# Performance work log

Hardware: AMD Instinct MI355X
Metric: run time of the kernel (lower is better)

The kernel has to match this reference:

```python
import jax, jax.numpy as jnp
import numpy as np

T, D, N, K, H, F = 2048, 4096, 32, 8, 128, 14336
THETA = 500000.0
EPS = 1e-5


def setup_inputs() -> dict:
    key = jax.random.key(0)
    ks = jax.random.split(key, 10)
    s = 0.02  # weight init scale
    return {
        "x": jax.random.normal(ks[0], (T, D), jnp.float32),
        "positions": jnp.arange(T, dtype=jnp.int32),
        "ln1_scale": jnp.ones((D,), jnp.float32),
        "w_q": jax.random.normal(ks[1], (D, N, H), jnp.float32) * s,
        "w_k": jax.random.normal(ks[2], (D, K, H), jnp.float32) * s,
        "w_v": jax.random.normal(ks[3], (D, K, H), jnp.float32) * s,
        "w_o": jax.random.normal(ks[4], (N, H, D), jnp.float32) * s,
        "ln2_scale": jnp.ones((D,), jnp.float32),
        "w_gate": jax.random.normal(ks[5], (D, F), jnp.float32) * s,
        "w_up": jax.random.normal(ks[6], (D, F), jnp.float32) * s,
        "w_down": jax.random.normal(ks[7], (F, D), jnp.float32) * s,
    }


def _rms_norm(x, scale):
    var = jnp.mean(jnp.square(x), axis=-1, keepdims=True)
    return x * jax.lax.rsqrt(var + EPS) * scale


def _apply_rope(x, pos):
    # x: [T, heads, H]; Llama rotate-half RoPE
    half = H // 2
    inv_freq = 1.0 / (THETA ** (jnp.arange(half, dtype=jnp.float32) / half))
    ang = pos.astype(jnp.float32)[:, None] * inv_freq[None, :]      # [T, half]
    cos = jnp.cos(ang)[:, None, :]
    sin = jnp.sin(ang)[:, None, :]
    x1, x2 = x[..., :half], x[..., half:]
    return jnp.concatenate([x1 * cos - x2 * sin, x2 * cos + x1 * sin], axis=-1)


def reference(x, positions, ln1_scale, w_q, w_k, w_v, w_o, ln2_scale, w_gate, w_up, w_down):
    # --- input RMSNorm ---
    h = _rms_norm(x, ln1_scale)
    # --- QKV projections + RoPE ---
    q = _apply_rope(jnp.einsum('td,dnh->tnh', h, w_q), positions)   # [T,N,H]
    k = _apply_rope(jnp.einsum('td,dkh->tkh', h, w_k), positions)   # [T,K,H]
    v = jnp.einsum('td,dkh->tkh', h, w_v)                            # [T,K,H]
    # --- GQA causal attention (prefill) ---
    G = N // K
    qg = q.reshape(T, K, G, H)
    scale = 1.0 / jnp.sqrt(jnp.float32(H))
    scores = jnp.einsum('tkgh,skh->kgts', qg, k) * scale             # [K,G,T,T]
    causal = positions[:, None] >= positions[None, :]                # [T,T]
    scores = jnp.where(causal[None, None], scores, jnp.finfo(scores.dtype).min)
    probs = jax.nn.softmax(scores, axis=-1)
    attn = jnp.einsum('kgts,skh->tkgh', probs, v).reshape(T, N, H)
    attn_out = jnp.einsum('tnh,nhd->td', attn, w_o)
    # --- residual ---
    residual = attn_out + x
    # --- post-attn RMSNorm + SwiGLU MLP ---
    h2 = _rms_norm(residual, ln2_scale)
    gate = jax.nn.silu(h2 @ w_gate)
    up = h2 @ w_up
    out = (gate * up) @ w_down
    return residual + out
```

## Files before the change

### kernel.cpp

```cpp
#include <hip/hip_runtime.h>

typedef __attribute__((ext_vector_type(8))) short bf16x8;
typedef __attribute__((ext_vector_type(4))) float f32x4;

constexpr int T = 2048;
constexpr int D = 4096;
constexpr int NQ = 32;
constexpr int NKV = 8;
constexpr int H = 128;
constexpr int F = 14336;
constexpr int NQKV = (NQ + 2 * NKV) * H;
constexpr int VOFF = (NQ + NKV) * H;

__device__ inline unsigned short f2bf(float f) {
  unsigned u = __float_as_uint(f);
  return (unsigned short)((u + 0x7FFFu + ((u >> 16) & 1u)) >> 16);
}

__device__ inline void gload_lds16(const void* g, void* l) {
  __builtin_amdgcn_global_load_lds((const __attribute__((address_space(1))) void*)g,
                                   (__attribute__((address_space(3))) void*)l, 16, 0, 0);
}

#define MFMA16(a, b, c) __builtin_amdgcn_mfma_f32_16x16x32_bf16(a, b, c, 0, 0, 0)

template <int MODE>
__global__ __launch_bounds__(256) void transpose_bf16(const float* __restrict__ in,
                                                      unsigned short* __restrict__ out,
                                                      int K, int N) {
  __shared__ float tile[64 * 65];
  const int kb = blockIdx.x * 64;
  const int nb = blockIdx.y * 64;
  const int tid = threadIdx.x;
  const int r = tid >> 2;
  const int c4 = tid & 3;
#pragma unroll
  for (int i = 0; i < 4; ++i) {
    float4 v = *(const float4*)(in + (size_t)(kb + r) * N + nb + c4 * 16 + i * 4);
    *(float4*)&tile[r * 65 + c4 * 16 + i * 4] = v;
  }
  __syncthreads();
  const int n = tid >> 2;
  const int kq = tid & 3;
  int nsrc = nb + n;
  int prow = (MODE == 0) ? nsrc : ((nsrc >> 4) * 32 + (nsrc & 15) + (MODE == 2 ? 16 : 0));
#pragma unroll
  for (int half = 0; half < 2; ++half) {
    ushort4 o0, o1;
    int k0 = kq * 16 + half * 8;
    o0.x = f2bf(tile[(k0 + 0) * 65 + n]);
    o0.y = f2bf(tile[(k0 + 1) * 65 + n]);
    o0.z = f2bf(tile[(k0 + 2) * 65 + n]);
    o0.w = f2bf(tile[(k0 + 3) * 65 + n]);
    o1.x = f2bf(tile[(k0 + 4) * 65 + n]);
    o1.y = f2bf(tile[(k0 + 5) * 65 + n]);
    o1.z = f2bf(tile[(k0 + 6) * 65 + n]);
    o1.w = f2bf(tile[(k0 + 7) * 65 + n]);
    unsigned short* op = out + (size_t)prow * K + kb + k0;
    *(ushort4*)(op + 0) = o0;
    *(ushort4*)(op + 4) = o1;
  }
}

__global__ __launch_bounds__(256) void rmsnorm_kernel(
    const float* __restrict__ in, const float* __restrict__ scale,
    unsigned short* __restrict__ out) {
  int row = blockIdx.x;
  const float4* xr = (const float4*)(in + (size_t)row * D);
  const float4* sr = (const float4*)scale;
  float4 vals[4];
  float ss = 0.f;
#pragma unroll
  for (int i = 0; i < 4; ++i) {
    float4 v = xr[threadIdx.x + i * 256];
    vals[i] = v;
    ss += v.x * v.x + v.y * v.y + v.z * v.z + v.w * v.w;
  }
#pragma unroll
  for (int off = 32; off; off >>= 1) ss += __shfl_xor(ss, off, 64);
  __shared__ float wsum[4];
  if ((threadIdx.x & 63) == 0) wsum[threadIdx.x >> 6] = ss;
  __syncthreads();
  float r = rsqrtf((wsum[0] + wsum[1] + wsum[2] + wsum[3]) * (1.f / D) + 1e-5f);
#pragma unroll
  for (int i = 0; i < 4; ++i) {
    int vi = threadIdx.x + i * 256;
    float4 v = vals[i];
    float4 s = sr[vi];
    ushort4 o;
    o.x = f2bf(v.x * r * s.x);
    o.y = f2bf(v.y * r * s.y);
    o.z = f2bf(v.z * r * s.z);
    o.w = f2bf(v.w * r * s.w);
    *(ushort4*)(out + (size_t)row * D + (size_t)vi * 4) = o;
  }
}

__global__ __launch_bounds__(256) void rmsnorm_add3(
    const float* __restrict__ a, const float* __restrict__ b,
    const float* __restrict__ c, const float* __restrict__ scale,
    float* __restrict__ residOut, unsigned short* __restrict__ out) {
  int row = blockIdx.x;
  const float4* ar = (const float4*)(a + (size_t)row * D);
  const float4* br = (const float4*)(b + (size_t)row * D);
  const float4* cr = (const float4*)(c + (size_t)row * D);
  const float4* sr = (const float4*)scale;
  float4* rr = (float4*)(residOut + (size_t)row * D);
  float4 vals[4];
  float ss = 0.f;
#pragma unroll
  for (int i = 0; i < 4; ++i) {
    int vi = threadIdx.x + i * 256;
    float4 va = ar[vi], vb = br[vi], vc = cr[vi];
    float4 v;
    v.x = va.x + vb.x + vc.x;
    v.y = va.y + vb.y + vc.y;
    v.z = va.z + vb.z + vc.z;
    v.w = va.w + vb.w + vc.w;
    vals[i] = v;
    ss += v.x * v.x + v.y * v.y + v.z * v.z + v.w * v.w;
  }
#pragma unroll
  for (int off = 32; off; off >>= 1) ss += __shfl_xor(ss, off, 64);
  __shared__ float wsum[4];
  if ((threadIdx.x & 63) == 0) wsum[threadIdx.x >> 6] = ss;
  __syncthreads();
  float r = rsqrtf((wsum[0] + wsum[1] + wsum[2] + wsum[3]) * (1.f / D) + 1e-5f);
#pragma unroll
  for (int i = 0; i < 4; ++i) {
    int vi = threadIdx.x + i * 256;
    float4 v = vals[i];
    rr[vi] = v;
    float4 s = sr[vi];
    ushort4 o;
    o.x = f2bf(v.x * r * s.x);
    o.y = f2bf(v.y * r * s.y);
    o.z = f2bf(v.z * r * s.z);
    o.w = f2bf(v.w * r * s.w);
    *(ushort4*)(out + (size_t)row * D + (size_t)vi * 4) = o;
  }
}

__global__ __launch_bounds__(256) void add3_kernel(const float* __restrict__ a,
                                                   const float* __restrict__ b,
                                                   const float* __restrict__ c,
                                                   float* __restrict__ o) {
  int i = blockIdx.x * 256 + threadIdx.x;
  float4 va = ((const float4*)a)[i];
  float4 vb = ((const float4*)b)[i];
  float4 vc = ((const float4*)c)[i];
  float4 vo;
  vo.x = va.x + vb.x + vc.x;
  vo.y = va.y + vb.y + vc.y;
  vo.z = va.z + vb.z + vc.z;
  vo.w = va.w + vb.w + vc.w;
  ((float4*)o)[i] = vo;
}

__global__ __launch_bounds__(256) void rope_table(const int* __restrict__ pos,
                                                  float* __restrict__ ctab,
                                                  float* __restrict__ stab) {
  int idx = blockIdx.x * 256 + threadIdx.x;
  int t = idx >> 6, i = idx & 63;
  float inv = exp2f(-(float)i * (log2f(500000.0f) / 64.0f));
  float ang = (float)pos[t] * inv;
  ctab[idx] = cosf(ang);
  stab[idx] = sinf(ang);
}

__global__ __launch_bounds__(256) void rope_bf16(const float* __restrict__ x,
                                                 const float* __restrict__ ctab,
                                                 const float* __restrict__ stab,
                                                 unsigned short* __restrict__ out,
                                                 int nheads, int row_stride, float scale) {
  int idx = blockIdx.x * 256 + threadIdx.x;
  int i = idx & 63;
  int tn = idx >> 6;
  int t = tn / nheads;
  int n = tn - t * nheads;
  float c = ctab[t * 64 + i], s = stab[t * 64 + i];
  const float* p = x + (size_t)t * row_stride + n * H;
  float x1 = p[i], x2 = p[i + 64];
  unsigned short* o = out + (size_t)tn * H;
  o[i] = f2bf((x1 * c - x2 * s) * scale);
  o[i + 64] = f2bf((x2 * c + x1 * s) * scale);
}

template <int EP>
__global__ __launch_bounds__(512, 2) void gemm256(
    const unsigned short* __restrict__ A, const unsigned short* __restrict__ Bt,
    float* __restrict__ outF, float* __restrict__ outF2,
    unsigned short* __restrict__ outB, int Kd, int Nd, int Klen) {
  __shared__ unsigned short lds[65536];
  const int tid = threadIdx.x, lane = tid & 63, wv = tid >> 6;
  const int wm = wv >> 2, wn = wv & 3;
  const int rl = lane & 15, g = lane >> 4;
  const int kz = blockIdx.z;
  int raw = blockIdx.x + blockIdx.y * gridDim.x;
  int cpx = (gridDim.x * gridDim.y) >> 3;
  int sid = (raw & 7) * cpx + (raw >> 3);
  int brow = sid % gridDim.x;
  int bcol = sid / gridDim.x;
  const int m0 = brow * 256, n0 = bcol * 256;

  const int l8 = lane >> 3;
  const int scol = ((lane & 7) ^ l8) * 8;
  const int xr = (rl & 7) << 4;
  const int pc0 = (g * 16) ^ xr;
  const int pc1 = (64 + g * 16) ^ xr;

  const char* ldsc = (const char*)lds;
  const unsigned short* gA = A + (size_t)(m0 + wv * 8 + l8) * Kd + kz * Klen + scol;
  const unsigned short* gB = Bt + (size_t)(n0 + wv * 8 + l8) * Kd + kz * Klen + scol;

  f32x4 acc[8][4];
#pragma unroll
  for (int i = 0; i < 8; ++i)
#pragma unroll
    for (int j = 0; j < 4; ++j) acc[i][j] = (f32x4){0.f, 0.f, 0.f, 0.f};

  const int NT = Klen >> 6;

#define STAGE_AL(kt, l)                                                      \
  gload_lds16(gA + (size_t)(kt) * 64 + (size_t)(l) * 64 * Kd,                \
              (void*)&lds[((kt) & 1) * 32768 + (l) * 4096 + wv * 512]);
#define STAGE_BL(kt, l)                                                      \
  gload_lds16(gB + (size_t)(kt) * 64 + (size_t)(l) * 64 * Kd,                \
              (void*)&lds[((kt) & 1) * 32768 + 16384 + (l) * 4096 + wv * 512]);
#define SBAR()                        \
  __builtin_amdgcn_sched_barrier(0);  \
  __builtin_amdgcn_s_barrier();

  STAGE_AL(0, 0); STAGE_AL(0, 1); STAGE_AL(0, 2); STAGE_AL(0, 3);
  STAGE_BL(0, 0); STAGE_BL(0, 1); STAGE_BL(0, 2); STAGE_BL(0, 3);
  STAGE_AL(1, 0); STAGE_AL(1, 1); STAGE_AL(1, 2); STAGE_AL(1, 3);
  STAGE_BL(1, 0); STAGE_BL(1, 1); STAGE_BL(1, 2); STAGE_BL(1, 3);
  asm volatile("s_waitcnt vmcnt(8)" ::: "memory");
  SBAR();

  const int bhalf = (wn >> 1) * 16384;
  const int brl = (wn & 1) * 64;

  bf16x8 bLoC[2][2];
  {
    const char* bB0 = ldsc + 32768 + bhalf;
#pragma unroll
    for (int nf = 0; nf < 2; ++nf) {
      bLoC[nf][0] = *(const bf16x8*)(bB0 + (brl + nf * 16 + rl) * 128 + pc0);
      bLoC[nf][1] = *(const bf16x8*)(bB0 + (brl + nf * 16 + rl) * 128 + pc1);
    }
  }

  for (int kt = 0; kt < NT; ++kt) {
    const int b = kt & 1;
    const char* aB = ldsc + b * 65536 + wm * 16384;
    const char* bB = ldsc + b * 65536 + 32768 + bhalf;
    const char* bBn = ldsc + (b ^ 1) * 65536 + 32768 + bhalf;
    const bool pre = (kt + 2 < NT);
    bf16x8 aLo[4][2], aHi[4][2], bHi[2][2], bLoN[2][2];
#pragma unroll
    for (int mf = 0; mf < 4; ++mf) {
      aLo[mf][0] = *(const bf16x8*)(aB + (mf * 16 + rl) * 128 + pc0);
      aLo[mf][1] = *(const bf16x8*)(aB + (mf * 16 + rl) * 128 + pc1);
    }
    SBAR();
    __builtin_amdgcn_s_setprio(1);
#pragma unroll
    for (int mf = 0; mf < 4; ++mf)
#pragma unroll
      for (int nf = 0; nf < 2; ++nf) {
        acc[mf][nf] = MFMA16(aLo[mf][0], bLoC[nf][0], acc[mf][nf]);
        acc[mf][nf] = MFMA16(aLo[mf][1], bLoC[nf][1], acc[mf][nf]);
      }
    __builtin_amdgcn_s_setprio(0);
#pragma unroll
    for (int nf = 0; nf < 2; ++nf) {
      bHi[nf][0] = *(const bf16x8*)(bB + (brl + (nf + 2) * 16 + rl) * 128 + pc0);
      bHi[nf][1] = *(const bf16x8*)(bB + (brl + (nf + 2) * 16 + rl) * 128 + pc1);
    }
    if (pre) { STAGE_AL(kt + 2, 0); STAGE_AL(kt + 2, 2); }
    SBAR();
    __builtin_amdgcn_s_setprio(1);
#pragma unroll
    for (int mf = 0; mf < 4; ++mf)
#pragma unroll
      for (int nf = 0; nf < 2; ++nf) {
        acc[mf][nf + 2] = MFMA16(aLo[mf][0], bHi[nf][0], acc[mf][nf + 2]);
        acc[mf][nf + 2] = MFMA16(aLo[mf][1], bHi[nf][1], acc[mf][nf + 2]);
      }
    __builtin_amdgcn_s_setprio(0);
#pragma unroll
    for (int mf = 0; mf < 4; ++mf) {
      aHi[mf][0] = *(const bf16x8*)(aB + ((mf + 4) * 16 + rl) * 128 + pc0);
      aHi[mf][1] = *(const bf16x8*)(aB + ((mf + 4) * 16 + rl) * 128 + pc1);
    }
    if (pre) {
      STAGE_BL(kt + 2, 0); STAGE_BL(kt + 2, 1);
      STAGE_BL(kt + 2, 2); STAGE_BL(kt + 2, 3);
      asm volatile("s_waitcnt vmcnt(6)" ::: "memory");
    } else {
      asm volatile("s_waitcnt vmcnt(0)" ::: "memory");
    }
    SBAR();
    __builtin_amdgcn_s_setprio(1);
#pragma unroll
    for (int mf = 0; mf < 4; ++mf)
#pragma unroll
      for (int nf = 0; nf < 2; ++nf) {
        acc[mf + 4][nf + 2] = MFMA16(aHi[mf][0], bHi[nf][0], acc[mf + 4][nf + 2]);
        acc[mf + 4][nf + 2] = MFMA16(aHi[mf][1], bHi[nf][1], acc[mf + 4][nf + 2]);
      }
    __builtin_amdgcn_s_setprio(0);
    if (pre) { STAGE_AL(kt + 2, 1); STAGE_AL(kt + 2, 3); }
    if (kt + 1 < NT) {
#pragma unroll
      for (int nf = 0; nf < 2; ++nf) {
        bLoN[nf][0] = *(const bf16x8*)(bBn + (brl + nf * 16 + rl) * 128 + pc0);
        bLoN[nf][1] = *(const bf16x8*)(bBn + (brl + nf * 16 + rl) * 128 + pc1);
      }
    }
    SBAR();
    __builtin_amdgcn_s_setprio(1);
#pragma unroll
    for (int mf = 0; mf < 4; ++mf)
#pragma unroll
      for (int nf = 0; nf < 2; ++nf) {
        acc[mf + 4][nf] = MFMA16(aHi[mf][0], bLoC[nf][0], acc[mf + 4][nf]);
        acc[mf + 4][nf] = MFMA16(aHi[mf][1], bLoC[nf][1], acc[mf + 4][nf]);
      }
    __builtin_amdgcn_s_setprio(0);
    if (kt + 1 < NT) {
#pragma unroll
      for (int nf = 0; nf < 2; ++nf) {
        bLoC[nf][0] = bLoN[nf][0];
        bLoC[nf][1] = bLoN[nf][1];
      }
    }
  }

  const int g4 = g * 4;
  if constexpr (EP == 5) {
    const int acolBase = ((n0 + wn * 64) >> 1) + rl;
#pragma unroll
    for (int mf = 0; mf < 8; ++mf)
#pragma unroll
      for (int p = 0; p < 2; ++p) {
        int acol = acolBase + p * 16;
#pragma unroll
        for (int jj = 0; jj < 4; ++jj) {
          int row = m0 + wm * 128 + mf * 16 + g4 + jj;
          float gg = acc[mf][2 * p][jj];
          float uu = acc[mf][2 * p + 1][jj];
          outB[(size_t)row * F + acol] = f2bf(gg / (1.f + __expf(-gg)) * uu);
        }
      }
  } else if constexpr (EP == 4) {
    if (n0 >= VOFF) {
#pragma unroll
      for (int mf = 0; mf < 8; ++mf)
#pragma unroll
        for (int q = 0; q < 4; ++q) {
          int col = n0 + wn * 64 + q * 16 + rl;
          int row0 = m0 + wm * 128 + mf * 16 + g4;
          ushort4 o;
          o.x = f2bf(acc[mf][q][0]);
          o.y = f2bf(acc[mf][q][1]);
          o.z = f2bf(acc[mf][q][2]);
          o.w = f2bf(acc[mf][q][3]);
          *(ushort4*)&outB[(size_t)(col - VOFF) * T + row0] = o;
        }
    } else {
#pragma unroll
      for (int mf = 0; mf < 8; ++mf)
#pragma unroll
        for (int q = 0; q < 4; ++q) {
          int col = n0 + wn * 64 + q * 16 + rl;
#pragma unroll
          for (int jj = 0; jj < 4; ++jj) {
            int row = m0 + wm * 128 + mf * 16 + g4 + jj;
            outF[(size_t)row * Nd + col] = acc[mf][q][jj];
          }
        }
    }
  } else {
    float* dst = kz ? outF2 : outF;
#pragma unroll
    for (int mf = 0; mf < 8; ++mf)
#pragma unroll
      for (int q = 0; q < 4; ++q) {
        int col = n0 + wn * 64 + q * 16 + rl;
#pragma unroll
        for (int jj = 0; jj < 4; ++jj) {
          int row = m0 + wm * 128 + mf * 16 + g4 + jj;
          dst[(size_t)row * Nd + col] = acc[mf][q][jj];
        }
      }
  }
#undef STAGE_AL
#undef STAGE_BL
#undef SBAR
}

constexpr int KLD = 136;
constexpr int VLD = 72;
constexpr int PLD = 72;

__global__ __launch_bounds__(512) void flash_attn(
    const unsigned short* __restrict__ qbf, const unsigned short* __restrict__ kbf,
    const unsigned short* __restrict__ vtbf, unsigned short* __restrict__ out) {
  __shared__ unsigned short K_lds[64 * KLD];
  __shared__ unsigned short Vt_lds[H * VLD];
  __shared__ unsigned short P_lds[8 * 16 * PLD];

  const int tid = threadIdx.x;
  const int lane = tid & 63;
  const int wv = tid >> 6;
  const int qb = blockIdx.x;
  const int kvh = blockIdx.y;
  const int qh = wv & 3, rh = wv >> 2;
  const int n = kvh * 4 + qh;
  const int g = lane >> 4;
  const int rl = lane & 15;
  const int qrow = qb * 32 + rh * 16;

  bf16x8 qfrag[4];
  {
    const unsigned short* qp = qbf + ((size_t)(qrow + rl) * NQ + n) * H + g * 8;
#pragma unroll
    for (int ks = 0; ks < 4; ++ks) qfrag[ks] = *(const bf16x8*)(qp + ks * 32);
  }

  f32x4 oacc[8];
#pragma unroll
  for (int ob = 0; ob < 8; ++ob) oacc[ob] = (f32x4){0.f, 0.f, 0.f, 0.f};
  float mrun[4] = {-1e30f, -1e30f, -1e30f, -1e30f};
  float lrun[4] = {0.f, 0.f, 0.f, 0.f};

  const int krow = tid >> 3, kseg = (tid & 7) * 16;
  const int vh = tid >> 2, vseg = (tid & 3) * 16;

  const int ktmax = (qb * 32 + 31) >> 6;
  for (int kt = 0; kt <= ktmax; ++kt) {
    const int kbase = kt * 64;
    __syncthreads();
    {
      const unsigned short* kp = kbf + ((size_t)(kbase + krow) * NKV + kvh) * H + kseg;
      *(bf16x8*)&K_lds[krow * KLD + kseg] = *(const bf16x8*)kp;
      *(bf16x8*)&K_lds[krow * KLD + kseg + 8] = *(const bf16x8*)(kp + 8);
      const unsigned short* vp = vtbf + (size_t)(kvh * H + vh) * T + kbase + vseg;
      *(bf16x8*)&Vt_lds[vh * VLD + vseg] = *(const bf16x8*)vp;
      *(bf16x8*)&Vt_lds[vh * VLD + vseg + 8] = *(const bf16x8*)(vp + 8);
    }
    __syncthreads();

    f32x4 sacc[4];
#pragma unroll
    for (int cb = 0; cb < 4; ++cb) sacc[cb] = (f32x4){0.f, 0.f, 0.f, 0.f};
#pragma unroll
    for (int cb = 0; cb < 4; ++cb)
#pragma unroll
      for (int ks = 0; ks < 4; ++ks) {
        bf16x8 kf = *(const bf16x8*)&K_lds[(cb * 16 + rl) * KLD + ks * 32 + g * 8];
        sacc[cb] = MFMA16(qfrag[ks], kf, sacc[cb]);
      }

    if (kt == ktmax) {
#pragma unroll
      for (int cb = 0; cb < 4; ++cb) {
        int kv_abs = kbase + cb * 16 + rl;
#pragma unroll
        for (int r = 0; r < 4; ++r) {
          if (kv_abs > qrow + g * 4 + r) sacc[cb][r] = -1e30f;
        }
      }
    }

    float mx[4], sm[4], corr[4];
#pragma unroll
    for (int r = 0; r < 4; ++r) {
      float m0 = fmaxf(fmaxf(sacc[0][r], sacc[1][r]), fmaxf(sacc[2][r], sacc[3][r]));
#pragma unroll
      for (int off = 1; off < 16; off <<= 1) m0 = fmaxf(m0, __shfl_xor(m0, off, 64));
      float nm = fmaxf(mrun[r], m0);
      corr[r] = __expf(mrun[r] - nm);
      mrun[r] = nm;
      mx[r] = nm;
    }
#pragma unroll
    for (int cb = 0; cb < 4; ++cb)
#pragma unroll
      for (int r = 0; r < 4; ++r) sacc[cb][r] = __expf(sacc[cb][r] - mx[r]);
#pragma unroll
    for (int r = 0; r < 4; ++r) {
      float s0 = sacc[0][r] + sacc[1][r] + sacc[2][r] + sacc[3][r];
#pragma unroll
      for (int off = 1; off < 16; off <<= 1) s0 += __shfl_xor(s0, off, 64);
      sm[r] = s0;
      lrun[r] = lrun[r] * corr[r] + sm[r];
    }
#pragma unroll
    for (int ob = 0; ob < 8; ++ob)
#pragma unroll
      for (int r = 0; r < 4; ++r) oacc[ob][r] *= corr[r];

#pragma unroll
    for (int cb = 0; cb < 4; ++cb)
#pragma unroll
      for (int r = 0; r < 4; ++r)
        P_lds[(wv * 16 + g * 4 + r) * PLD + cb * 16 + rl] = f2bf(sacc[cb][r]);

    bf16x8 pa[2];
#pragma unroll
    for (int ks = 0; ks < 2; ++ks)
      pa[ks] = *(const bf16x8*)&P_lds[(wv * 16 + rl) * PLD + ks * 32 + g * 8];

#pragma unroll
    for (int ob = 0; ob < 8; ++ob)
#pragma unroll
      for (int ks = 0; ks < 2; ++ks) {
        bf16x8 vf = *(const bf16x8*)&Vt_lds[(ob * 16 + rl) * VLD + ks * 32 + g * 8];
        oacc[ob] = MFMA16(pa[ks], vf, oacc[ob]);
      }
  }

  float inv[4];
#pragma unroll
  for (int r = 0; r < 4; ++r) inv[r] = 1.f / lrun[r];
#pragma unroll
  for (int ob = 0; ob < 8; ++ob)
#pragma unroll
    for (int r = 0; r < 4; ++r) {
      int t = qrow + g * 4 + r;
      out[((size_t)t * NQ + n) * H + ob * 16 + rl] = f2bf(oacc[ob][r] * inv[r]);
    }
}

extern "C" void kernel_launch(void* const* d_in, const int* in_sizes, int n_in,
                              void* d_out, int out_size, void* d_ws, size_t ws_size,
                              hipStream_t stream) {
  (void)in_sizes; (void)n_in; (void)out_size; (void)ws_size;
  const float* x = (const float*)d_in[0];
  const int* positions = (const int*)d_in[1];
  const float* ln1 = (const float*)d_in[2];
  const float* w_q = (const float*)d_in[3];
  const float* w_k = (const float*)d_in[4];
  const float* w_v = (const float*)d_in[5];
  const float* w_o = (const float*)d_in[6];
  const float* ln2 = (const float*)d_in[7];
  const float* w_gate = (const float*)d_in[8];
  const float* w_up = (const float*)d_in[9];
  const float* w_down = (const float*)d_in[10];
  float* out = (float*)d_out;

  char* ws = (char*)d_ws;
  size_t off = 0;
  auto alloc = [&](size_t bytes) {
    char* p = ws + off;
    off += (bytes + 255) & ~(size_t)255;
    return p;
  };
  unsigned short* h_bf = (unsigned short*)alloc((size_t)T * D * 2);
  unsigned short* h2_bf = (unsigned short*)alloc((size_t)T * D * 2);
  unsigned short* attn_bf = (unsigned short*)alloc((size_t)T * NQ * H * 2);
  unsigned short* act_bf = (unsigned short*)alloc((size_t)T * F * 2);
  float* qkvf = (float*)alloc((size_t)T * NQKV * 4);
  float* resid = (float*)alloc((size_t)T * D * 4);
  float* ctab = (float*)alloc((size_t)T * 64 * 4);
  float* stab = (float*)alloc((size_t)T * 64 * 4);
  unsigned short* qbf = (unsigned short*)alloc((size_t)T * NQ * H * 2);
  unsigned short* kbf = (unsigned short*)alloc((size_t)T * NKV * H * 2);
  unsigned short* vtbf = (unsigned short*)alloc((size_t)NKV * H * T * 2);
  unsigned short* wqkvt = (unsigned short*)alloc((size_t)NQKV * D * 2);
  unsigned short* wot = (unsigned short*)alloc((size_t)D * NQ * H * 2);
  unsigned short* wgut = (unsigned short*)alloc((size_t)2 * F * D * 2);
  unsigned short* wdt = (unsigned short*)alloc((size_t)D * F * 2);
  float* part0 = qkvf;
  float* part1 = (float*)wqkvt;

  transpose_bf16<0><<<dim3(D / 64, (NQ * H) / 64), 256, 0, stream>>>(w_q, wqkvt, D, NQ * H);
  transpose_bf16<0><<<dim3(D / 64, (NKV * H) / 64), 256, 0, stream>>>(
      w_k, wqkvt + (size_t)NQ * H * D, D, NKV * H);
  transpose_bf16<0><<<dim3(D / 64, (NKV * H) / 64), 256, 0, stream>>>(
      w_v, wqkvt + (size_t)VOFF * D, D, NKV * H);
  transpose_bf16<0><<<dim3((NQ * H) / 64, D / 64), 256, 0, stream>>>(w_o, wot, NQ * H, D);
  transpose_bf16<1><<<dim3(D / 64, F / 64), 256, 0, stream>>>(w_gate, wgut, D, F);
  transpose_bf16<2><<<dim3(D / 64, F / 64), 256, 0, stream>>>(w_up, wgut, D, F);
  transpose_bf16<0><<<dim3(F / 64, D / 64), 256, 0, stream>>>(w_down, wdt, F, D);

  rmsnorm_kernel<<<T, 256, 0, stream>>>(x, ln1, h_bf);
  rope_table<<<(T * 64) / 256, 256, 0, stream>>>(positions, ctab, stab);
  gemm256<4><<<dim3(T / 256, NQKV / 256, 1), 512, 0, stream>>>(
      h_bf, wqkvt, qkvf, nullptr, vtbf, D, NQKV, D);
  rope_bf16<<<(T * NQ * 64) / 256, 256, 0, stream>>>(qkvf, ctab, stab, qbf, NQ, NQKV,
                                                     0.08838834764831845f);
  rope_bf16<<<(T * NKV * 64) / 256, 256, 0, stream>>>(qkvf + NQ * H, ctab, stab, kbf,
                                                      NKV, NQKV, 1.0f);
  flash_attn<<<dim3(T / 32, NKV), 512, 0, stream>>>(qbf, kbf, vtbf, attn_bf);
  gemm256<0><<<dim3(T / 256, D / 256, 2), 512, 0, stream>>>(
      attn_bf, wot, part0, part1, nullptr, NQ * H, D, NQ * H / 2);
  rmsnorm_add3<<<T, 256, 0, stream>>>(part0, part1, x, ln2, resid, h2_bf);
  gemm256<5><<<dim3(T / 256, (2 * F) / 256), 512, 0, stream>>>(
      h2_bf, wgut, nullptr, nullptr, act_bf, D, 2 * F, D);
  gemm256<0><<<dim3(T / 256, D / 256, 2), 512, 0, stream>>>(
      act_bf, wdt, part0, part1, nullptr, F, D, F / 2);
  add3_kernel<<<(T * D / 4) / 256, 256, 0, stream>>>(part0, part1, resid, out);
}
```

Measured before the change: 1.283 ms.

## Switch GEMM to 32x32x16 MFMA tiles and prefetch flash-attn K/V tiles into registers

The 256x256 GEMM now uses 32x32x16 bf16 MFMA instead of 16x16x32. This cuts the count of LDS fragment reads and MFMA instructions per tile and reorders accumulators into f32x16. The gate/up weight interleave moves from 16-column to 32-column blocks to match, and the epilogues are remapped. Launch bounds drop to one block per CU, since the larger register footprint may not fit two. Flash attention now loads the next K/V tile into registers while the current tile is processed, hiding global load latency at the cost of more registers.

```diff
diff --git a/kernel.cpp b/kernel.cpp
--- a/kernel.cpp
+++ b/kernel.cpp
@@ -2,6 +2,7 @@
 
 typedef __attribute__((ext_vector_type(8))) short bf16x8;
 typedef __attribute__((ext_vector_type(4))) float f32x4;
+typedef __attribute__((ext_vector_type(16))) float f32x16;
 
 constexpr int T = 2048;
 constexpr int D = 4096;
@@ -23,6 +24,7 @@
 }
 
 #define MFMA16(a, b, c) __builtin_amdgcn_mfma_f32_16x16x32_bf16(a, b, c, 0, 0, 0)
+#define MFMA32(a, b, c) __builtin_amdgcn_mfma_f32_32x32x16_bf16(a, b, c, 0, 0, 0)
 
 template <int MODE>
 __global__ __launch_bounds__(256) void transpose_bf16(const float* __restrict__ in,
@@ -43,7 +45,7 @@
   const int n = tid >> 2;
   const int kq = tid & 3;
   int nsrc = nb + n;
-  int prow = (MODE == 0) ? nsrc : ((nsrc >> 4) * 32 + (nsrc & 15) + (MODE == 2 ? 16 : 0));
+  int prow = (MODE == 0) ? nsrc : ((nsrc >> 5) * 64 + (nsrc & 31) + (MODE == 2 ? 32 : 0));
 #pragma unroll
   for (int half = 0; half < 2; ++half) {
     ushort4 o0, o1;
@@ -187,14 +189,14 @@
 }
 
 template <int EP>
-__global__ __launch_bounds__(512, 2) void gemm256(
+__global__ __launch_bounds__(512, 1) void gemm256(
     const unsigned short* __restrict__ A, const unsigned short* __restrict__ Bt,
     float* __restrict__ outF, float* __restrict__ outF2,
     unsigned short* __restrict__ outB, int Kd, int Nd, int Klen) {
   __shared__ unsigned short lds[65536];
   const int tid = threadIdx.x, lane = tid & 63, wv = tid >> 6;
   const int wm = wv >> 2, wn = wv & 3;
-  const int rl = lane & 15, g = lane >> 4;
+  const int r32 = lane & 31, h = lane >> 5;
   const int kz = blockIdx.z;
   int raw = blockIdx.x + blockIdx.y * gridDim.x;
   int cpx = (gridDim.x * gridDim.y) >> 3;
@@ -205,19 +207,20 @@
 
   const int l8 = lane >> 3;
   const int scol = ((lane & 7) ^ l8) * 8;
-  const int xr = (rl & 7) << 4;
-  const int pc0 = (g * 16) ^ xr;
-  const int pc1 = (64 + g * 16) ^ xr;
+  const int xr = (r32 & 7) << 4;
+  int pc[4];
+#pragma unroll
+  for (int ks = 0; ks < 4; ++ks) pc[ks] = (ks * 32 + h * 16) ^ xr;
 
   const char* ldsc = (const char*)lds;
   const unsigned short* gA = A + (size_t)(m0 + wv * 8 + l8) * Kd + kz * Klen + scol;
   const unsigned short* gB = Bt + (size_t)(n0 + wv * 8 + l8) * Kd + kz * Klen + scol;
 
-  f32x4 acc[8][4];
-#pragma unroll
-  for (int i = 0; i < 8; ++i)
-#pragma unroll
-    for (int j = 0; j < 4; ++j) acc[i][j] = (f32x4){0.f, 0.f, 0.f, 0.f};
+  f32x16 acc[4][2];
+#pragma unroll
+  for (int i = 0; i < 4; ++i)
+#pragma unroll
+    for (int j = 0; j < 2; ++j) acc[i][j] = (f32x16)(0.f);
 
   const int NT = Klen >> 6;
 
@@ -238,62 +241,50 @@
   asm volatile("s_waitcnt vmcnt(8)" ::: "memory");
   SBAR();
 
-  const int bhalf = (wn >> 1) * 16384;
-  const int brl = (wn & 1) * 64;
-
-  bf16x8 bLoC[2][2];
+  bf16x8 bLoC[4];
   {
-    const char* bB0 = ldsc + 32768 + bhalf;
-#pragma unroll
-    for (int nf = 0; nf < 2; ++nf) {
-      bLoC[nf][0] = *(const bf16x8*)(bB0 + (brl + nf * 16 + rl) * 128 + pc0);
-      bLoC[nf][1] = *(const bf16x8*)(bB0 + (brl + nf * 16 + rl) * 128 + pc1);
-    }
+    const char* bB0 = ldsc + 32768 + (wn * 64 + r32) * 128;
+#pragma unroll
+    for (int ks = 0; ks < 4; ++ks) bLoC[ks] = *(const bf16x8*)(bB0 + pc[ks]);
   }
 
   for (int kt = 0; kt < NT; ++kt) {
     const int b = kt & 1;
-    const char* aB = ldsc + b * 65536 + wm * 16384;
-    const char* bB = ldsc + b * 65536 + 32768 + bhalf;
-    const char* bBn = ldsc + (b ^ 1) * 65536 + 32768 + bhalf;
+    const char* aB = ldsc + b * 65536 + (wm * 128 + r32) * 128;
+    const char* bB = ldsc + b * 65536 + 32768 + (wn * 64 + r32) * 128;
+    const char* bBn = ldsc + (b ^ 1) * 65536 + 32768 + (wn * 64 + r32) * 128;
     const bool pre = (kt + 2 < NT);
-    bf16x8 aLo[4][2], aHi[4][2], bHi[2][2], bLoN[2][2];
-#pragma unroll
-    for (int mf = 0; mf < 4; ++mf) {
-      aLo[mf][0] = *(const bf16x8*)(aB + (mf * 16 + rl) * 128 + pc0);
-      aLo[mf][1] = *(const bf16x8*)(aB + (mf * 16 + rl) * 128 + pc1);
-    }
+    bf16x8 aCur[2][4], aHi[2][4], bHi[4], bLoN[4];
+#pragma unroll
+    for (int mp = 0; mp < 2; ++mp)
+#pragma unroll
+      for (int ks = 0; ks < 4; ++ks)
+        aCur[mp][ks] = *(const bf16x8*)(aB + mp * 32 * 128 + pc[ks]);
     SBAR();
     __builtin_amdgcn_s_setprio(1);
 #pragma unroll
-    for (int mf = 0; mf < 4; ++mf)
-#pragma unroll
-      for (int nf = 0; nf < 2; ++nf) {
-        acc[mf][nf] = MFMA16(aLo[mf][0], bLoC[nf][0], acc[mf][nf]);
-        acc[mf][nf] = MFMA16(aLo[mf][1], bLoC[nf][1], acc[mf][nf]);
-      }
+    for (int mp = 0; mp < 2; ++mp)
+#pragma unroll
+      for (int ks = 0; ks < 4; ++ks)
+        acc[mp][0] = MFMA32(aCur[mp][ks], bLoC[ks], acc[mp][0]);
     __builtin_amdgcn_s_setprio(0);
 #pragma unroll
-    for (int nf = 0; nf < 2; ++nf) {
-      bHi[nf][0] = *(const bf16x8*)(bB + (brl + (nf + 2) * 16 + rl) * 128 + pc0);
-      bHi[nf][1] = *(const bf16x8*)(bB + (brl + (nf + 2) * 16 + rl) * 128 + pc1);
-    }
+    for (int ks = 0; ks < 4; ++ks)
+      bHi[ks] = *(const bf16x8*)(bB + 32 * 128 + pc[ks]);
     if (pre) { STAGE_AL(kt + 2, 0); STAGE_AL(kt + 2, 2); }
     SBAR();
     __builtin_amdgcn_s_setprio(1);
 #pragma unroll
-    for (int mf = 0; mf < 4; ++mf)
-#pragma unroll
-      for (int nf = 0; nf < 2; ++nf) {
-        acc[mf][nf + 2] = MFMA16(aLo[mf][0], bHi[nf][0], acc[mf][nf + 2]);
-        acc[mf][nf + 2] = MFMA16(aLo[mf][1], bHi[nf][1], acc[mf][nf + 2]);
-      }
+    for (int mp = 0; mp < 2; ++mp)
+#pragma unroll
+      for (int ks = 0; ks < 4; ++ks)
+        acc[mp][1] = MFMA32(aCur[mp][ks], bHi[ks], acc[mp][1]);
     __builtin_amdgcn_s_setprio(0);
 #pragma unroll
-    for (int mf = 0; mf < 4; ++mf) {
-      aHi[mf][0] = *(const bf16x8*)(aB + ((mf + 4) * 16 + rl) * 128 + pc0);
-      aHi[mf][1] = *(const bf16x8*)(aB + ((mf + 4) * 16 + rl) * 128 + pc1);
-    }
+    for (int mp = 0; mp < 2; ++mp)
+#pragma unroll
+      for (int ks = 0; ks < 4; ++ks)
+        aHi[mp][ks] = *(const bf16x8*)(aB + (64 + mp * 32) * 128 + pc[ks]);
     if (pre) {
       STAGE_BL(kt + 2, 0); STAGE_BL(kt + 2, 1);
       STAGE_BL(kt + 2, 2); STAGE_BL(kt + 2, 3);
@@ -304,96 +295,84 @@
     SBAR();
     __builtin_amdgcn_s_setprio(1);
 #pragma unroll
-    for (int mf = 0; mf < 4; ++mf)
-#pragma unroll
-      for (int nf = 0; nf < 2; ++nf) {
-        acc[mf + 4][nf + 2] = MFMA16(aHi[mf][0], bHi[nf][0], acc[mf + 4][nf + 2]);
-        acc[mf + 4][nf + 2] = MFMA16(aHi[mf][1], bHi[nf][1], acc[mf + 4][nf + 2]);
-      }
+    for (int mp = 0; mp < 2; ++mp)
+#pragma unroll
+      for (int ks = 0; ks < 4; ++ks)
+        acc[2 + mp][1] = MFMA32(aHi[mp][ks], bHi[ks], acc[2 + mp][1]);
     __builtin_amdgcn_s_setprio(0);
     if (pre) { STAGE_AL(kt + 2, 1); STAGE_AL(kt + 2, 3); }
     if (kt + 1 < NT) {
 #pragma unroll
-      for (int nf = 0; nf < 2; ++nf) {
-        bLoN[nf][0] = *(const bf16x8*)(bBn + (brl + nf * 16 + rl) * 128 + pc0);
-        bLoN[nf][1] = *(const bf16x8*)(bBn + (brl + nf * 16 + rl) * 128 + pc1);
-      }
+      for (int ks = 0; ks < 4; ++ks) bLoN[ks] = *(const bf16x8*)(bBn + pc[ks]);
     }
     SBAR();
     __builtin_amdgcn_s_setprio(1);
 #pragma unroll
-    for (int mf = 0; mf < 4; ++mf)
-#pragma unroll
-      for (int nf = 0; nf < 2; ++nf) {
-        acc[mf + 4][nf] = MFMA16(aHi[mf][0], bLoC[nf][0], acc[mf + 4][nf]);
-        acc[mf + 4][nf] = MFMA16(aHi[mf][1], bLoC[nf][1], acc[mf + 4][nf]);
-      }
+    for (int mp = 0; mp < 2; ++mp)
+#pragma unroll
+      for (int ks = 0; ks < 4; ++ks)
+        acc[2 + mp][0] = MFMA32(aHi[mp][ks], bLoC[ks], acc[2 + mp][0]);
     __builtin_amdgcn_s_setprio(0);
     if (kt + 1 < NT) {
 #pragma unroll
-      for (int nf = 0; nf < 2; ++nf) {
-        bLoC[nf][0] = bLoN[nf][0];
-        bLoC[nf][1] = bLoN[nf][1];
+      for (int ks = 0; ks < 4; ++ks) bLoC[ks] = bLoN[ks];
+    }
+  }
+
+  if constexpr (EP == 5) {
+    const int acol = ((n0 + wn * 64) >> 1) + r32;
+#pragma unroll
+    for (int mf = 0; mf < 4; ++mf) {
+      int rowb = m0 + wm * 128 + mf * 32 + 4 * h;
+#pragma unroll
+      for (int r = 0; r < 16; ++r) {
+        int row = rowb + (r & 3) + 8 * (r >> 2);
+        float gg = acc[mf][0][r];
+        float uu = acc[mf][1][r];
+        outB[(size_t)row * F + acol] = f2bf(gg / (1.f + __expf(-gg)) * uu);
       }
     }
-  }
-
-  const int g4 = g * 4;
-  if constexpr (EP == 5) {
-    const int acolBase = ((n0 + wn * 64) >> 1) + rl;
-#pragma unroll
-    for (int mf = 0; mf < 8; ++mf)
-#pragma unroll
-      for (int p = 0; p < 2; ++p) {
-        int acol = acolBase + p * 16;
-#pragma unroll
-        for (int jj = 0; jj < 4; ++jj) {
-          int row = m0 + wm * 128 + mf * 16 + g4 + jj;
-          float gg = acc[mf][2 * p][jj];
-          float uu = acc[mf][2 * p + 1][jj];
-          outB[(size_t)row * F + acol] = f2bf(gg / (1.f + __expf(-gg)) * uu);
-        }
-      }
   } else if constexpr (EP == 4) {
     if (n0 >= VOFF) {
 #pragma unroll
-      for (int mf = 0; mf < 8; ++mf)
-#pragma unroll
-        for (int q = 0; q < 4; ++q) {
-          int col = n0 + wn * 64 + q * 16 + rl;
-          int row0 = m0 + wm * 128 + mf * 16 + g4;
-          ushort4 o;
-          o.x = f2bf(acc[mf][q][0]);
-          o.y = f2bf(acc[mf][q][1]);
-          o.z = f2bf(acc[mf][q][2]);
-          o.w = f2bf(acc[mf][q][3]);
-          *(ushort4*)&outB[(size_t)(col - VOFF) * T + row0] = o;
+      for (int mf = 0; mf < 4; ++mf)
+#pragma unroll
+        for (int nf = 0; nf < 2; ++nf) {
+          int col = n0 + wn * 64 + nf * 32 + r32;
+          int rowb = m0 + wm * 128 + mf * 32 + 4 * h;
+#pragma unroll
+          for (int q = 0; q < 4; ++q) {
+            ushort4 o;
+            o.x = f2bf(acc[mf][nf][q * 4 + 0]);
+            o.y = f2bf(acc[mf][nf][q * 4 + 1]);
+            o.z = f2bf(acc[mf][nf][q * 4 + 2]);
+            o.w = f2bf(acc[mf][nf][q * 4 + 3]);
+            *(ushort4*)&outB[(size_t)(col - VOFF) * T + rowb + 8 * q] = o;
+          }
         }
     } else {
 #pragma unroll
-      for (int mf = 0; mf < 8; ++mf)
-#pragma unroll
-        for (int q = 0; q < 4; ++q) {
-          int col = n0 + wn * 64 + q * 16 + rl;
-#pragma unroll
-          for (int jj = 0; jj < 4; ++jj) {
-            int row = m0 + wm * 128 + mf * 16 + g4 + jj;
-            outF[(size_t)row * Nd + col] = acc[mf][q][jj];
-          }
+      for (int mf = 0; mf < 4; ++mf)
+#pragma unroll
+        for (int nf = 0; nf < 2; ++nf) {
+          int col = n0 + wn * 64 + nf * 32 + r32;
+          int rowb = m0 + wm * 128 + mf * 32 + 4 * h;
+#pragma unroll
+          for (int r = 0; r < 16; ++r)
+            outF[(size_t)(rowb + (r & 3) + 8 * (r >> 2)) * Nd + col] = acc[mf][nf][r];
         }
     }
   } else {
     float* dst = kz ? outF2 : outF;
 #pragma unroll
-    for (int mf = 0; mf < 8; ++mf)
-#pragma unroll
-      for (int q = 0; q < 4; ++q) {
-        int col = n0 + wn * 64 + q * 16 + rl;
-#pragma unroll
-        for (int jj = 0; jj < 4; ++jj) {
-          int row = m0 + wm * 128 + mf * 16 + g4 + jj;
-          dst[(size_t)row * Nd + col] = acc[mf][q][jj];
-        }
+    for (int mf = 0; mf < 4; ++mf)
+#pragma unroll
+      for (int nf = 0; nf < 2; ++nf) {
+        int col = n0 + wn * 64 + nf * 32 + r32;
+        int rowb = m0 + wm * 128 + mf * 32 + 4 * h;
+#pragma unroll
+        for (int r = 0; r < 16; ++r)
+          dst[(size_t)(rowb + (r & 3) + 8 * (r >> 2)) * Nd + col] = acc[mf][nf][r];
       }
   }
 #undef STAGE_AL
@@ -440,16 +419,31 @@
   const int vh = tid >> 2, vseg = (tid & 3) * 16;
 
   const int ktmax = (qb * 32 + 31) >> 6;
+  bf16x8 krA, krB, vrA, vrB;
+  {
+    const unsigned short* kp = kbf + ((size_t)krow * NKV + kvh) * H + kseg;
+    krA = *(const bf16x8*)kp;
+    krB = *(const bf16x8*)(kp + 8);
+    const unsigned short* vp = vtbf + (size_t)(kvh * H + vh) * T + vseg;
+    vrA = *(const bf16x8*)vp;
+    vrB = *(const bf16x8*)(vp + 8);
+  }
   for (int kt = 0; kt <= ktmax; ++kt) {
     const int kbase = kt * 64;
     __syncthreads();
-    {
-      const unsigned short* kp = kbf + ((size_t)(kbase + krow) * NKV + kvh) * H + kseg;
-      *(bf16x8*)&K_lds[krow * KLD + kseg] = *(const bf16x8*)kp;
-      *(bf16x8*)&K_lds[krow * KLD + kseg + 8] = *(const bf16x8*)(kp + 8);
-      const unsigned short* vp = vtbf + (size_t)(kvh * H + vh) * T + kbase + vseg;
-      *(bf16x8*)&Vt_lds[vh * VLD + vseg] = *(const bf16x8*)vp;
-      *(bf16x8*)&Vt_lds[vh * VLD + vseg + 8] = *(const bf16x8*)(vp + 8);
+    *(bf16x8*)&K_lds[krow * KLD + kseg] = krA;
+    *(bf16x8*)&K_lds[krow * KLD + kseg + 8] = krB;
+    *(bf16x8*)&Vt_lds[vh * VLD + vseg] = vrA;
+    *(bf16x8*)&Vt_lds[vh * VLD + vseg + 8] = vrB;
+    if (kt < ktmax) {
+      const unsigned short* kp =
+          kbf + ((size_t)(kbase + 64 + krow) * NKV + kvh) * H + kseg;
+      krA = *(const bf16x8*)kp;
+      krB = *(const bf16x8*)(kp + 8);
+      const unsigned short* vp =
+          vtbf + (size_t)(kvh * H + vh) * T + kbase + 64 + vseg;
+      vrA = *(const bf16x8*)vp;
+      vrB = *(const bf16x8*)(vp + 8);
     }
     __syncthreads();
 
```

Result: slower. 1.366 ms (+6.5%).

## Flatten GEMM K-loop into single MFMA phase and register-prefetch attention K/V tiles

Applied to the files above, without the earlier changes.

The 256x256 GEMM main loop drops its four-phase interleaved schedule, which split LDS fragment reads, async global-to-LDS staging and MFMAs across several barriers. It now loads all A/B fragments up front, issues all staging loads for tile kt+2, then runs all 64 MFMAs. Launch bounds go from 2 to 1 waves per SIMD to leave room for the larger register footprint, giving up occupancy. Separately, the attention kernel now prefetches the next K/V tile into registers while the current tile is in LDS, hiding global load latency behind compute.

```diff
diff --git a/kernel.cpp b/kernel.cpp
--- a/kernel.cpp
+++ b/kernel.cpp
@@ -187,7 +187,7 @@
 }
 
 template <int EP>
-__global__ __launch_bounds__(512, 2) void gemm256(
+__global__ __launch_bounds__(512, 1) void gemm256(
     const unsigned short* __restrict__ A, const unsigned short* __restrict__ Bt,
     float* __restrict__ outF, float* __restrict__ outF2,
     unsigned short* __restrict__ outB, int Kd, int Nd, int Klen) {
@@ -241,101 +241,44 @@
   const int bhalf = (wn >> 1) * 16384;
   const int brl = (wn & 1) * 64;
 
-  bf16x8 bLoC[2][2];
-  {
-    const char* bB0 = ldsc + 32768 + bhalf;
-#pragma unroll
-    for (int nf = 0; nf < 2; ++nf) {
-      bLoC[nf][0] = *(const bf16x8*)(bB0 + (brl + nf * 16 + rl) * 128 + pc0);
-      bLoC[nf][1] = *(const bf16x8*)(bB0 + (brl + nf * 16 + rl) * 128 + pc1);
-    }
-  }
-
   for (int kt = 0; kt < NT; ++kt) {
     const int b = kt & 1;
     const char* aB = ldsc + b * 65536 + wm * 16384;
     const char* bB = ldsc + b * 65536 + 32768 + bhalf;
-    const char* bBn = ldsc + (b ^ 1) * 65536 + 32768 + bhalf;
     const bool pre = (kt + 2 < NT);
-    bf16x8 aLo[4][2], aHi[4][2], bHi[2][2], bLoN[2][2];
-#pragma unroll
-    for (int mf = 0; mf < 4; ++mf) {
-      aLo[mf][0] = *(const bf16x8*)(aB + (mf * 16 + rl) * 128 + pc0);
-      aLo[mf][1] = *(const bf16x8*)(aB + (mf * 16 + rl) * 128 + pc1);
+    bf16x8 aR[8][2], bR[4][2];
+#pragma unroll
+    for (int mf = 0; mf < 8; ++mf) {
+      aR[mf][0] = *(const bf16x8*)(aB + (mf * 16 + rl) * 128 + pc0);
+      aR[mf][1] = *(const bf16x8*)(aB + (mf * 16 + rl) * 128 + pc1);
+    }
+#pragma unroll
+    for (int nf = 0; nf < 4; ++nf) {
+      bR[nf][0] = *(const bf16x8*)(bB + (brl + nf * 16 + rl) * 128 + pc0);
+      bR[nf][1] = *(const bf16x8*)(bB + (brl + nf * 16 + rl) * 128 + pc1);
     }
     SBAR();
+    if (pre) {
+      STAGE_AL(kt + 2, 0); STAGE_AL(kt + 2, 1);
+      STAGE_AL(kt + 2, 2); STAGE_AL(kt + 2, 3);
+      STAGE_BL(kt + 2, 0); STAGE_BL(kt + 2, 1);
+      STAGE_BL(kt + 2, 2); STAGE_BL(kt + 2, 3);
+    }
     __builtin_amdgcn_s_setprio(1);
 #pragma unroll
-    for (int mf = 0; mf < 4; ++mf)
-#pragma unroll
-      for (int nf = 0; nf < 2; ++nf) {
-        acc[mf][nf] = MFMA16(aLo[mf][0], bLoC[nf][0], acc[mf][nf]);
-        acc[mf][nf] = MFMA16(aLo[mf][1], bLoC[nf][1], acc[mf][nf]);
+    for (int mf = 0; mf < 8; ++mf)
+#pragma unroll
+      for (int nf = 0; nf < 4; ++nf) {
+        acc[mf][nf] = MFMA16(aR[mf][0], bR[nf][0], acc[mf][nf]);
+        acc[mf][nf] = MFMA16(aR[mf][1], bR[nf][1], acc[mf][nf]);
       }
     __builtin_amdgcn_s_setprio(0);
-#pragma unroll
-    for (int nf = 0; nf < 2; ++nf) {
-      bHi[nf][0] = *(const bf16x8*)(bB + (brl + (nf + 2) * 16 + rl) * 128 + pc0);
-      bHi[nf][1] = *(const bf16x8*)(bB + (brl + (nf + 2) * 16 + rl) * 128 + pc1);
-    }
-    if (pre) { STAGE_AL(kt + 2, 0); STAGE_AL(kt + 2, 2); }
+    if (pre) {
+      asm volatile("s_waitcnt vmcnt(8)" ::: "memory");
+    } else if (kt + 1 < NT) {
+      asm volatile("s_waitcnt vmcnt(0)" ::: "memory");
+    }
     SBAR();
-    __builtin_amdgcn_s_setprio(1);
-#pragma unroll
-    for (int mf = 0; mf < 4; ++mf)
-#pragma unroll
-      for (int nf = 0; nf < 2; ++nf) {
-        acc[mf][nf + 2] = MFMA16(aLo[mf][0], bHi[nf][0], acc[mf][nf + 2]);
-        acc[mf][nf + 2] = MFMA16(aLo[mf][1], bHi[nf][1], acc[mf][nf + 2]);
-      }
-    __builtin_amdgcn_s_setprio(0);
-#pragma unroll
-    for (int mf = 0; mf < 4; ++mf) {
-      aHi[mf][0] = *(const bf16x8*)(aB + ((mf + 4) * 16 + rl) * 128 + pc0);
-      aHi[mf][1] = *(const bf16x8*)(aB + ((mf + 4) * 16 + rl) * 128 + pc1);
-    }
-    if (pre) {
-      STAGE_BL(kt + 2, 0); STAGE_BL(kt + 2, 1);
-      STAGE_BL(kt + 2, 2); STAGE_BL(kt + 2, 3);
-      asm volatile("s_waitcnt vmcnt(6)" ::: "memory");
-    } else {
-      asm volatile("s_waitcnt vmcnt(0)" ::: "memory");
-    }
-    SBAR();
-    __builtin_amdgcn_s_setprio(1);
-#pragma unroll
-    for (int mf = 0; mf < 4; ++mf)
-#pragma unroll
-      for (int nf = 0; nf < 2; ++nf) {
-        acc[mf + 4][nf + 2] = MFMA16(aHi[mf][0], bHi[nf][0], acc[mf + 4][nf + 2]);
-        acc[mf + 4][nf + 2] = MFMA16(aHi[mf][1], bHi[nf][1], acc[mf + 4][nf + 2]);
-      }
-    __builtin_amdgcn_s_setprio(0);
-    if (pre) { STAGE_AL(kt + 2, 1); STAGE_AL(kt + 2, 3); }
-    if (kt + 1 < NT) {
-#pragma unroll
-      for (int nf = 0; nf < 2; ++nf) {
-        bLoN[nf][0] = *(const bf16x8*)(bBn + (brl + nf * 16 + rl) * 128 + pc0);
-        bLoN[nf][1] = *(const bf16x8*)(bBn + (brl + nf * 16 + rl) * 128 + pc1);
-      }
-    }
-    SBAR();
-    __builtin_amdgcn_s_setprio(1);
-#pragma unroll
-    for (int mf = 0; mf < 4; ++mf)
-#pragma unroll
-      for (int nf = 0; nf < 2; ++nf) {
-        acc[mf + 4][nf] = MFMA16(aHi[mf][0], bLoC[nf][0], acc[mf + 4][nf]);
-        acc[mf + 4][nf] = MFMA16(aHi[mf][1], bLoC[nf][1], acc[mf + 4][nf]);
-      }
-    __builtin_amdgcn_s_setprio(0);
-    if (kt + 1 < NT) {
-#pragma unroll
-      for (int nf = 0; nf < 2; ++nf) {
-        bLoC[nf][0] = bLoN[nf][0];
-        bLoC[nf][1] = bLoN[nf][1];
-      }
-    }
   }
 
   const int g4 = g * 4;
@@ -440,16 +383,31 @@
   const int vh = tid >> 2, vseg = (tid & 3) * 16;
 
   const int ktmax = (qb * 32 + 31) >> 6;
+  bf16x8 krA, krB, vrA, vrB;
+  {
+    const unsigned short* kp = kbf + ((size_t)krow * NKV + kvh) * H + kseg;
+    krA = *(const bf16x8*)kp;
+    krB = *(const bf16x8*)(kp + 8);
+    const unsigned short* vp = vtbf + (size_t)(kvh * H + vh) * T + vseg;
+    vrA = *(const bf16x8*)vp;
+    vrB = *(const bf16x8*)(vp + 8);
+  }
   for (int kt = 0; kt <= ktmax; ++kt) {
     const int kbase = kt * 64;
     __syncthreads();
-    {
-      const unsigned short* kp = kbf + ((size_t)(kbase + krow) * NKV + kvh) * H + kseg;
-      *(bf16x8*)&K_lds[krow * KLD + kseg] = *(const bf16x8*)kp;
-      *(bf16x8*)&K_lds[krow * KLD + kseg + 8] = *(const bf16x8*)(kp + 8);
-      const unsigned short* vp = vtbf + (size_t)(kvh * H + vh) * T + kbase + vseg;
-      *(bf16x8*)&Vt_lds[vh * VLD + vseg] = *(const bf16x8*)vp;
-      *(bf16x8*)&Vt_lds[vh * VLD + vseg + 8] = *(const bf16x8*)(vp + 8);
+    *(bf16x8*)&K_lds[krow * KLD + kseg] = krA;
+    *(bf16x8*)&K_lds[krow * KLD + kseg + 8] = krB;
+    *(bf16x8*)&Vt_lds[vh * VLD + vseg] = vrA;
+    *(bf16x8*)&Vt_lds[vh * VLD + vseg + 8] = vrB;
+    if (kt < ktmax) {
+      const unsigned short* kp =
+          kbf + ((size_t)(kbase + 64 + krow) * NKV + kvh) * H + kseg;
+      krA = *(const bf16x8*)kp;
+      krB = *(const bf16x8*)(kp + 8);
+      const unsigned short* vp =
+          vtbf + (size_t)(kvh * H + vh) * T + kbase + 64 + vseg;
+      vrA = *(const bf16x8*)vp;
+      vrB = *(const bf16x8*)(vp + 8);
     }
     __syncthreads();
 
```

Measured after the change: 1.331 ms. 1.04x slower.

## Store Q/K projections as bf16 and register-prefetch next K/V tile in attention

Applied to the files above, without the earlier changes.

The QKV GEMM epilogue now writes the Q and K columns as bf16 with a compact row stride instead of fp32, and the RoPE kernel reads bf16 input, halving that intermediate traffic. The flash attention loop prefetches the next K/V tile into registers while the current one is staged in LDS, overlapping global load latency with compute. This adds an extra bf16 rounding before RoPE, which slightly changes numerics, and raises register pressure in the attention kernel.

```diff
diff --git a/kernel.cpp b/kernel.cpp
--- a/kernel.cpp
+++ b/kernel.cpp
@@ -15,6 +15,10 @@
 __device__ inline unsigned short f2bf(float f) {
   unsigned u = __float_as_uint(f);
   return (unsigned short)((u + 0x7FFFu + ((u >> 16) & 1u)) >> 16);
+}
+
+__device__ inline float bf2f(unsigned short u) {
+  return __uint_as_float((unsigned)u << 16);
 }
 
 __device__ inline void gload_lds16(const void* g, void* l) {
@@ -168,7 +172,7 @@
   stab[idx] = sinf(ang);
 }
 
-__global__ __launch_bounds__(256) void rope_bf16(const float* __restrict__ x,
+__global__ __launch_bounds__(256) void rope_bf16(const unsigned short* __restrict__ x,
                                                  const float* __restrict__ ctab,
                                                  const float* __restrict__ stab,
                                                  unsigned short* __restrict__ out,
@@ -179,8 +183,8 @@
   int t = tn / nheads;
   int n = tn - t * nheads;
   float c = ctab[t * 64 + i], s = stab[t * 64 + i];
-  const float* p = x + (size_t)t * row_stride + n * H;
-  float x1 = p[i], x2 = p[i + 64];
+  const unsigned short* p = x + (size_t)t * row_stride + n * H;
+  float x1 = bf2f(p[i]), x2 = bf2f(p[i + 64]);
   unsigned short* o = out + (size_t)tn * H;
   o[i] = f2bf((x1 * c - x2 * s) * scale);
   o[i + 64] = f2bf((x2 * c + x1 * s) * scale);
@@ -370,6 +374,7 @@
           *(ushort4*)&outB[(size_t)(col - VOFF) * T + row0] = o;
         }
     } else {
+      unsigned short* qk = (unsigned short*)outF;
 #pragma unroll
       for (int mf = 0; mf < 8; ++mf)
 #pragma unroll
@@ -378,7 +383,7 @@
 #pragma unroll
           for (int jj = 0; jj < 4; ++jj) {
             int row = m0 + wm * 128 + mf * 16 + g4 + jj;
-            outF[(size_t)row * Nd + col] = acc[mf][q][jj];
+            qk[(size_t)row * VOFF + col] = f2bf(acc[mf][q][jj]);
           }
         }
     }
@@ -440,16 +445,31 @@
   const int vh = tid >> 2, vseg = (tid & 3) * 16;
 
   const int ktmax = (qb * 32 + 31) >> 6;
+  bf16x8 krA, krB, vrA, vrB;
+  {
+    const unsigned short* kp = kbf + ((size_t)krow * NKV + kvh) * H + kseg;
+    krA = *(const bf16x8*)kp;
+    krB = *(const bf16x8*)(kp + 8);
+    const unsigned short* vp = vtbf + (size_t)(kvh * H + vh) * T + vseg;
+    vrA = *(const bf16x8*)vp;
+    vrB = *(const bf16x8*)(vp + 8);
+  }
   for (int kt = 0; kt <= ktmax; ++kt) {
     const int kbase = kt * 64;
     __syncthreads();
-    {
-      const unsigned short* kp = kbf + ((size_t)(kbase + krow) * NKV + kvh) * H + kseg;
-      *(bf16x8*)&K_lds[krow * KLD + kseg] = *(const bf16x8*)kp;
-      *(bf16x8*)&K_lds[krow * KLD + kseg + 8] = *(const bf16x8*)(kp + 8);
-      const unsigned short* vp = vtbf + (size_t)(kvh * H + vh) * T + kbase + vseg;
-      *(bf16x8*)&Vt_lds[vh * VLD + vseg] = *(const bf16x8*)vp;
-      *(bf16x8*)&Vt_lds[vh * VLD + vseg + 8] = *(const bf16x8*)(vp + 8);
+    *(bf16x8*)&K_lds[krow * KLD + kseg] = krA;
+    *(bf16x8*)&K_lds[krow * KLD + kseg + 8] = krB;
+    *(bf16x8*)&Vt_lds[vh * VLD + vseg] = vrA;
+    *(bf16x8*)&Vt_lds[vh * VLD + vseg + 8] = vrB;
+    if (kt < ktmax) {
+      const unsigned short* kp =
+          kbf + ((size_t)(kbase + 64 + krow) * NKV + kvh) * H + kseg;
+      krA = *(const bf16x8*)kp;
+      krB = *(const bf16x8*)(kp + 8);
+      const unsigned short* vp =
+          vtbf + (size_t)(kvh * H + vh) * T + kbase + 64 + vseg;
+      vrA = *(const bf16x8*)vp;
+      vrB = *(const bf16x8*)(vp + 8);
     }
     __syncthreads();
 
@@ -576,6 +596,7 @@
   unsigned short* wdt = (unsigned short*)alloc((size_t)D * F * 2);
   float* part0 = qkvf;
   float* part1 = (float*)wqkvt;
+  unsigned short* qkbf = (unsigned short*)qkvf;
 
   transpose_bf16<0><<<dim3(D / 64, (NQ * H) / 64), 256, 0, stream>>>(w_q, wqkvt, D, NQ * H);
   transpose_bf16<0><<<dim3(D / 64, (NKV * H) / 64), 256, 0, stream>>>(
@@ -591,10 +612,10 @@
   rope_table<<<(T * 64) / 256, 256, 0, stream>>>(positions, ctab, stab);
   gemm256<4><<<dim3(T / 256, NQKV / 256, 1), 512, 0, stream>>>(
       h_bf, wqkvt, qkvf, nullptr, vtbf, D, NQKV, D);
-  rope_bf16<<<(T * NQ * 64) / 256, 256, 0, stream>>>(qkvf, ctab, stab, qbf, NQ, NQKV,
+  rope_bf16<<<(T * NQ * 64) / 256, 256, 0, stream>>>(qkbf, ctab, stab, qbf, NQ, VOFF,
                                                      0.08838834764831845f);
-  rope_bf16<<<(T * NKV * 64) / 256, 256, 0, stream>>>(qkvf + NQ * H, ctab, stab, kbf,
-                                                      NKV, NQKV, 1.0f);
+  rope_bf16<<<(T * NKV * 64) / 256, 256, 0, stream>>>(qkbf + NQ * H, ctab, stab, kbf,
+                                                      NKV, VOFF, 1.0f);
   flash_attn<<<dim3(T / 32, NKV), 512, 0, stream>>>(qbf, kbf, vtbf, attn_bf);
   gemm256<0><<<dim3(T / 256, D / 256, 2), 512, 0, stream>>>(
       attn_bf, wot, part0, part1, nullptr, NQ * H, D, NQ * H / 2);
```

Result: no change. 1.285 ms, median of 3 (+0.1%).
